# Kernel tuning notes

Measured on AMD Instinct MI355X. Metric: run time of the kernel, lower is better.

Reference implementation:

```python
import jax, jax.numpy as jnp
import numpy as np

B, NB, K = 8, 2000, 5          # batch, num_blockneuron, groups (reservoir = NB*K)
R = NB * K                      # reservoir_num = 10000
DIN = 400                       # per-input feature dim; fc in_dim = 5*DIN
DECAY = 0.5
REF = 0.5
THR_BASE1, THR_BETA1 = 0.1, 0.07
CUR_BASE1, CUR_BETA1 = 0.05, 0.07
WSCALE = 0.02


def setup_inputs() -> dict:
    key = jax.random.key(0)
    ks = jax.random.split(key, 11)
    inp = {}
    for i in range(5):
        inp[f"in{i+1}"] = jax.random.normal(ks[i], (B, DIN), dtype=jnp.float32)
    inp["W_fc"] = jax.random.normal(ks[5], (R, 5 * DIN), dtype=jnp.float32) * WSCALE
    inp["b_fc"] = jax.random.normal(ks[6], (R,), dtype=jnp.float32) * WSCALE
    inp["W_fv"] = jax.random.normal(ks[7], (R, R), dtype=jnp.float32) * WSCALE
    inp["b_fv"] = jax.random.normal(ks[8], (R,), dtype=jnp.float32) * WSCALE
    inp["W_mlp"] = jax.random.normal(ks[9], (100, R), dtype=jnp.float32) * WSCALE
    inp["b_mlp"] = jax.random.normal(ks[10], (100,), dtype=jnp.float32) * WSCALE
    return inp


def reference(in1, in2, in3, in4, in5, W_fc, b_fc, W_fv, b_fv, W_mlp, b_mlp):
    x = jnp.concatenate([in1, in2, in3, in4, in5], axis=1)  # (B, 2000)
    # traces start at zero on the first step -> thr/cur are the base values
    thr = THR_BASE1
    cur = CUR_BASE1
    spike0 = jnp.zeros((B, R), dtype=x.dtype)
    mem0 = jnp.zeros((B, R), dtype=x.dtype)

    # wta_mem_update
    state = x @ W_fc.T + b_fc + spike0 @ W_fv.T + b_fv          # (B, R)
    mem = (mem0 - spike0 * REF) * DECAY + state + cur           # (B, R)
    mem = mem.reshape(B, NB, K)                                  # (B, NB, K)
    # sort descending over the block dim; only order stats 159/160 are needed
    topq, _ = jax.lax.top_k(mem.transpose(0, 2, 1), 161)        # (B, K, 161)
    mem_q1 = topq[..., 160]                                      # 161st largest
    mem_q2 = topq[..., 159]                                      # 160th largest
    nps = (mem_q1 + (mem_q2 - mem_q1) * 0.2)[:, None, :]         # (B, 1, K)
    mem = jax.nn.relu(mem - nps).reshape(B, -1)                  # (B, R)
    spike = (mem - thr > 0).astype(jnp.float32)                  # (B, R)

    r_sumspike = spike                                           # 0 + spike
    out = spike @ W_mlp.T + b_mlp                                # (B, 100)
    return out, r_sumspike
```

## Files before the change

### kernel.cpp

```cpp
#include <hip/hip_runtime.h>

#define BB   8
#define NBL  2000
#define RR   10000
#define XDIM 2000

template <int CTRL>
__device__ __forceinline__ float dpp_add(float v) {
    int s = __builtin_amdgcn_update_dpp(0, __float_as_int(v), CTRL, 0xf, 0xf, true);
    return v + __int_as_float(s);
}

__global__ __launch_bounds__(256, 4) void kA_gemm(
    const float* __restrict__ in1, const float* __restrict__ in2,
    const float* __restrict__ in3, const float* __restrict__ in4,
    const float* __restrict__ in5,
    const float* __restrict__ Wfc, const float* __restrict__ bfc,
    const float* __restrict__ bfv, float* __restrict__ mem2,
    unsigned* __restrict__ counter)
{
    if (blockIdx.x == 0 && threadIdx.x == 0) *counter = 0u;

    const int tid  = threadIdx.x;
    const int wave = tid >> 6, lane = tid & 63;
    const int nb    = blockIdx.x;
    const int rbase = nb * 5;

    float acc[5][BB];
    #pragma unroll
    for (int q = 0; q < 5; ++q)
        #pragma unroll
        for (int b = 0; b < BB; ++b) acc[q][b] = 0.f;

    #pragma unroll
    for (int i = 0; i < 2; ++i) {
        const int col = wave * 512 + i * 256 + (lane << 2);
        const bool valid = col < XDIM;
        const int wh  = col / 400;
        const int off = col - wh * 400;
        const float* xp = in1;
        xp = (wh == 1) ? in2 : xp;
        xp = (wh == 2) ? in3 : xp;
        xp = (wh == 3) ? in4 : xp;
        xp = (wh == 4) ? in5 : xp;

        float4 w[5];
        #pragma unroll
        for (int q = 0; q < 5; ++q)
            w[q] = valid ? *(const float4*)(Wfc + (size_t)(rbase + q) * XDIM + col)
                         : make_float4(0.f, 0.f, 0.f, 0.f);

        #pragma unroll
        for (int b = 0; b < BB; ++b) {
            float4 xv = valid ? *(const float4*)(xp + b * 400 + off)
                              : make_float4(0.f, 0.f, 0.f, 0.f);
            #pragma unroll
            for (int q = 0; q < 5; ++q)
                acc[q][b] += w[q].x * xv.x + w[q].y * xv.y + w[q].z * xv.z + w[q].w * xv.w;
        }
    }

    __shared__ float part[4][5][BB];
    #pragma unroll
    for (int q = 0; q < 5; ++q) {
        #pragma unroll
        for (int b = 0; b < BB; ++b) {
            float v = acc[q][b];
            v = dpp_add<0xB1>(v);
            v = dpp_add<0x4E>(v);
            v = dpp_add<0x141>(v);
            v = dpp_add<0x140>(v);
            v = dpp_add<0x142>(v);
            v = dpp_add<0x143>(v);
            if (lane == 63) part[wave][q][b] = v;
        }
    }
    __syncthreads();

    if (wave == 0 && lane < 40) {
        const int q = lane >> 3, b = lane & 7;
        const int r = rbase + q;
        const float v = part[0][q][b] + part[1][q][b] + part[2][q][b] + part[3][q][b];
        mem2[(q * BB + b) * NBL + nb] = v + bfc[r] + bfv[r] + 0.05f;
    }
}

__device__ __forceinline__ unsigned sortkey(float f) {
    unsigned u = __float_as_uint(f);
    return (u & 0x80000000u) ? ~u : (u | 0x80000000u);
}
__device__ __forceinline__ float unsortkey(unsigned u) {
    unsigned ub = (u & 0x80000000u) ? (u ^ 0x80000000u) : ~u;
    return __uint_as_float(ub);
}

__global__ __launch_bounds__(512) void kB_spike_out(
    const float* __restrict__ mem2, const float* __restrict__ Wmlp,
    const float* __restrict__ bmlp, float* __restrict__ spike_out,
    float* __restrict__ out, unsigned* __restrict__ counter,
    unsigned long long* __restrict__ maskws)
{
    __shared__ float wlds[RR];
    __shared__ float red[8][BB];
    const int tid = threadIdx.x;
    const int blk = blockIdx.x;
    const bool is_sel = (blk < 40) && (tid < 64);

    if (!is_sel) {
        const int nstage = (blk < 40) ? 448 : 512;
        const int stid   = (blk < 40) ? (tid - 64) : tid;
        for (int j = stid; j < 2500; j += nstage) {
            const int col = j * 4;
            *(float4*)&wlds[col] = *(const float4*)(Wmlp + (size_t)blk * RR + col);
        }
    }

    if (is_sel) {
        const int b = blk / 5, k = blk - b * 5;
        const int lane = tid;
        const float* src = mem2 + (k * BB + b) * NBL;

        float    f[32];
        unsigned u[32];
        #pragma unroll
        for (int i = 0; i < 32; ++i) {
            int nb = i * 64 + lane;
            f[i] = (nb < NBL) ? src[nb] : 0.f;
            u[i] = (nb < NBL) ? sortkey(f[i]) : 0u;
        }

        unsigned X = 0;
        for (int bit = 31; bit >= 0; --bit) {
            unsigned cand = X | (1u << bit);
            int c = 0;
            #pragma unroll
            for (int i = 0; i < 32; ++i)
                c += (int)__popcll(__ballot(u[i] >= cand));
            if (c >= 160) X = cand;
        }
        const unsigned q2u = X;

        int cge = 0;
        #pragma unroll
        for (int i = 0; i < 32; ++i)
            cge += (int)__popcll(__ballot(u[i] >= q2u));

        unsigned q1u;
        if (cge >= 161) {
            q1u = q2u;
        } else {
            unsigned m = 0;
            #pragma unroll
            for (int i = 0; i < 32; ++i)
                if (u[i] < q2u && u[i] > m) m = u[i];
            #pragma unroll
            for (int o = 32; o >= 1; o >>= 1) {
                unsigned ot = __shfl_xor(m, o, 64);
                m = (ot > m) ? ot : m;
            }
            q1u = m;
        }

        const float q2 = unsortkey(q2u), q1 = unsortkey(q1u);
        const float nps = q1 + (q2 - q1) * 0.2f;

        unsigned long long* maskp = maskws + blk * 32;
        #pragma unroll
        for (int i = 0; i < 32; ++i) {
            int nb = i * 64 + lane;
            const bool sp = (nb < NBL) && (f[i] - nps > 0.1f);
            const unsigned long long m = __ballot(sp);
            if (nb < NBL)
                spike_out[b * RR + nb * 5 + k] = sp ? 1.0f : 0.0f;
            if (lane == 0) maskp[i] = m;
        }
        __threadfence();
        if (lane == 0) atomicAdd(counter, 1u);
    }

    __syncthreads();
    if (tid == 0) {
        while (__hip_atomic_load(counter, __ATOMIC_ACQUIRE, __HIP_MEMORY_SCOPE_AGENT) < 40u)
            __builtin_amdgcn_s_sleep(2);
        __threadfence();
    }
    __syncthreads();

    const int o = blk;
    const int wave = tid >> 6, lane = tid & 63;

    float acc[BB];
    #pragma unroll
    for (int b = 0; b < BB; ++b) acc[b] = 0.f;

    for (int c = wave; c < 32; c += 8) {
        const int nb  = c * 64 + lane;
        const int nbc = (nb < NBL) ? nb : (NBL - 1);
        const float* wp5 = &wlds[nbc * 5];
        #pragma unroll
        for (int k = 0; k < 5; ++k) {
            const float wk = wp5[k];
            #pragma unroll
            for (int b = 0; b < BB; ++b) {
                const unsigned long long m = maskws[(b * 5 + k) * 32 + c];
                acc[b] += (((unsigned)(m >> lane)) & 1u) ? wk : 0.f;
            }
        }
    }

    #pragma unroll
    for (int b = 0; b < BB; ++b) {
        float v = acc[b];
        v = dpp_add<0xB1>(v);
        v = dpp_add<0x4E>(v);
        v = dpp_add<0x141>(v);
        v = dpp_add<0x140>(v);
        v = dpp_add<0x142>(v);
        v = dpp_add<0x143>(v);
        if (lane == 63) red[wave][b] = v;
    }
    __syncthreads();
    if (tid < BB) {
        float v = 0.f;
        #pragma unroll
        for (int w = 0; w < 8; ++w) v += red[w][tid];
        out[tid * 100 + o] = v + bmlp[o];
    }
}

extern "C" void kernel_launch(void* const* d_in, const int* in_sizes, int n_in,
                              void* d_out, int out_size, void* d_ws, size_t ws_size,
                              hipStream_t stream) {
    const float* in1  = (const float*)d_in[0];
    const float* in2  = (const float*)d_in[1];
    const float* in3  = (const float*)d_in[2];
    const float* in4  = (const float*)d_in[3];
    const float* in5  = (const float*)d_in[4];
    const float* Wfc  = (const float*)d_in[5];
    const float* bfc  = (const float*)d_in[6];
    const float* bfv  = (const float*)d_in[8];
    const float* Wmlp = (const float*)d_in[9];
    const float* bmlp = (const float*)d_in[10];

    float* out   = (float*)d_out;
    float* spike = out + 800;

    float*    mem2    = (float*)d_ws;
    unsigned* counter = (unsigned*)((char*)d_ws + 80000 * sizeof(float));
    unsigned long long* maskws =
        (unsigned long long*)((char*)d_ws + 80000 * sizeof(float) + 16);

    kA_gemm<<<2000, 256, 0, stream>>>(in1, in2, in3, in4, in5, Wfc, bfc, bfv,
                                      mem2, counter);
    kB_spike_out<<<100, 512, 0, stream>>>(mem2, Wmlp, bmlp, spike, out, counter,
                                          maskws);
}
```

Baseline: 57.68 us.

## Publish per-group thresholds and recompute spikes in all blocks instead of bitmasks

The 40 selection waves now publish only their threshold value per (batch, group) rather than writing spike outputs and 64-bit ballot masks. After the grid-wide barrier, every block re-reads mem2 with float4 loads, compares against the shared thresholds and accumulates Wmlp weights. Blocks under 40 also write the spike output using 500 threads instead of one wave. This shortens the serial critical path in the selection wave, at the cost of redundant mem2 reads (80K floats per block across 100 blocks, mostly L2 hits) and strided scattered spike stores.

```diff
diff --git a/kernel.cpp b/kernel.cpp
--- a/kernel.cpp
+++ b/kernel.cpp
@@ -98,10 +98,11 @@
     const float* __restrict__ mem2, const float* __restrict__ Wmlp,
     const float* __restrict__ bmlp, float* __restrict__ spike_out,
     float* __restrict__ out, unsigned* __restrict__ counter,
-    unsigned long long* __restrict__ maskws)
+    float* __restrict__ npsws)
 {
     __shared__ float wlds[RR];
     __shared__ float red[8][BB];
+    __shared__ float npslds[40];
     const int tid = threadIdx.x;
     const int blk = blockIdx.x;
     const bool is_sel = (blk < 40) && (tid < 64);
@@ -164,16 +165,7 @@
         const float q2 = unsortkey(q2u), q1 = unsortkey(q1u);
         const float nps = q1 + (q2 - q1) * 0.2f;
 
-        unsigned long long* maskp = maskws + blk * 32;
-        #pragma unroll
-        for (int i = 0; i < 32; ++i) {
-            int nb = i * 64 + lane;
-            const bool sp = (nb < NBL) && (f[i] - nps > 0.1f);
-            const unsigned long long m = __ballot(sp);
-            if (nb < NBL)
-                spike_out[b * RR + nb * 5 + k] = sp ? 1.0f : 0.0f;
-            if (lane == 0) maskp[i] = m;
-        }
+        if (lane == 0) npsws[blk] = nps;
         __threadfence();
         if (lane == 0) atomicAdd(counter, 1u);
     }
@@ -186,6 +178,22 @@
     }
     __syncthreads();
 
+    if (tid < 40) npslds[tid] = npsws[tid];
+    __syncthreads();
+
+    if (blk < 40) {
+        const int b = blk / 5, k = blk - b * 5;
+        const float nps = npslds[blk];
+        if (tid < 500) {
+            const float4 v = *(const float4*)(mem2 + (k * BB + b) * NBL + tid * 4);
+            float* dst = spike_out + b * RR + (tid * 4) * 5 + k;
+            dst[0]  = (v.x - nps > 0.1f) ? 1.0f : 0.0f;
+            dst[5]  = (v.y - nps > 0.1f) ? 1.0f : 0.0f;
+            dst[10] = (v.z - nps > 0.1f) ? 1.0f : 0.0f;
+            dst[15] = (v.w - nps > 0.1f) ? 1.0f : 0.0f;
+        }
+    }
+
     const int o = blk;
     const int wave = tid >> 6, lane = tid & 63;
 
@@ -193,17 +201,23 @@
     #pragma unroll
     for (int b = 0; b < BB; ++b) acc[b] = 0.f;
 
-    for (int c = wave; c < 32; c += 8) {
-        const int nb  = c * 64 + lane;
-        const int nbc = (nb < NBL) ? nb : (NBL - 1);
-        const float* wp5 = &wlds[nbc * 5];
+    if (tid < 500) {
+        const int nb0 = tid * 4;
+        float wk[20];
+        #pragma unroll
+        for (int t = 0; t < 5; ++t)
+            *(float4*)&wk[t * 4] = *(const float4*)&wlds[nb0 * 5 + t * 4];
+
         #pragma unroll
         for (int k = 0; k < 5; ++k) {
-            const float wk = wp5[k];
             #pragma unroll
             for (int b = 0; b < BB; ++b) {
-                const unsigned long long m = maskws[(b * 5 + k) * 32 + c];
-                acc[b] += (((unsigned)(m >> lane)) & 1u) ? wk : 0.f;
+                const float4 v = *(const float4*)(mem2 + (k * BB + b) * NBL + nb0);
+                const float nps = npslds[b * 5 + k];
+                acc[b] += (v.x - nps > 0.1f) ? wk[0 * 5 + k] : 0.f;
+                acc[b] += (v.y - nps > 0.1f) ? wk[1 * 5 + k] : 0.f;
+                acc[b] += (v.z - nps > 0.1f) ? wk[2 * 5 + k] : 0.f;
+                acc[b] += (v.w - nps > 0.1f) ? wk[3 * 5 + k] : 0.f;
             }
         }
     }
@@ -247,11 +261,10 @@
 
     float*    mem2    = (float*)d_ws;
     unsigned* counter = (unsigned*)((char*)d_ws + 80000 * sizeof(float));
-    unsigned long long* maskws =
-        (unsigned long long*)((char*)d_ws + 80000 * sizeof(float) + 16);
+    float*    npsws   = (float*)((char*)d_ws + 80000 * sizeof(float) + 16);
 
     kA_gemm<<<2000, 256, 0, stream>>>(in1, in2, in3, in4, in5, Wfc, bfc, bfv,
                                       mem2, counter);
     kB_spike_out<<<100, 512, 0, stream>>>(mem2, Wmlp, bmlp, spike, out, counter,
-                                          maskws);
-}
+                                          npsws);
+}
```

Measured after the change: 54.07 us. -6.3%, faster.
